# Kernel optimization log

Measured on AMD Instinct MI355X. Metric: run time of the kernel, lower is better.

## Reference

```python
import jax, jax.numpy as jnp
import numpy as np

N_HEADS = 16


def setup_inputs() -> dict:
    key = jax.random.key(0)
    k1, k2, k3 = jax.random.split(key, 3)
    B, T, D = 2, 2048, 1024
    x = jax.random.normal(k1, (B, T, D), dtype=jnp.float32)
    w_qkv = jax.random.normal(k2, (3 * D, D), dtype=jnp.float32) * 0.02
    w_proj = jax.random.normal(k3, (D, D), dtype=jnp.float32) * (0.02 / np.sqrt(24.0))
    return {"x": x, "w_qkv": w_qkv, "w_proj": w_proj}


def reference(x, w_qkv, w_proj):
    B, T, D = x.shape
    H = N_HEADS
    dh = D // H
    # qkv linear (no bias): x @ w_qkv.T -> [B, T, 3D]
    qkv = jnp.einsum('btd,ed->bte', x, w_qkv)
    q, k, v = jnp.split(qkv, 3, axis=-1)
    q = q.reshape(B, T, H, dh)
    k = k.reshape(B, T, H, dh)
    v = v.reshape(B, T, H, dh)
    # attention with materialized scores [B, H, T, S]
    scores = jnp.einsum('bthd,bshd->bhts', q, k) / jnp.sqrt(jnp.asarray(dh, x.dtype))
    attn = jax.nn.softmax(scores.astype(jnp.float32), axis=-1).astype(x.dtype)
    out = jnp.einsum('bhts,bshd->bthd', attn, v).reshape(B, T, D)
    # output projection (no bias)
    return jnp.einsum('btd,ed->bte', out, w_proj)
```

## Files before the change

### kernel.cpp

```cpp
#include <hip/hip_runtime.h>


typedef __attribute__((ext_vector_type(8))) short s8v;
typedef __attribute__((ext_vector_type(8))) unsigned short us8;
typedef __attribute__((ext_vector_type(4))) float f4v;
typedef __attribute__((ext_vector_type(16))) float f16v;

__device__ __forceinline__ unsigned short f2b(float f) {
    unsigned u = __builtin_bit_cast(unsigned, f);
    u += 0x7FFFu + ((u >> 16) & 1u);
    return (unsigned short)(u >> 16);
}
__device__ __forceinline__ unsigned pack2(float a, float b) {
    unsigned ua = __builtin_bit_cast(unsigned, a);
    ua += 0x7FFFu + ((ua >> 16) & 1u);
    unsigned ub = __builtin_bit_cast(unsigned, b);
    ub += 0x7FFFu + ((ub >> 16) & 1u);
    return (ua >> 16) | (ub & 0xFFFF0000u);
}

#if __has_builtin(__builtin_amdgcn_exp2f)
#define EXP2F(x) __builtin_amdgcn_exp2f(x)
#else
#define EXP2F(x) exp2f(x)
#endif

#define QSCALE 0.18033688011112042f

__global__ __launch_bounds__(256) void cvt_all(const float* __restrict__ x,
                                               const float* __restrict__ wq,
                                               const float* __restrict__ wp,
                                               unsigned short* __restrict__ xb,
                                               unsigned short* __restrict__ wqb,
                                               unsigned short* __restrict__ wpb) {
    const int nx = 4096 * 1024 / 4, nq = 3072 * 1024 / 4;
    int i = blockIdx.x * 256 + threadIdx.x;
    const float* s;
    unsigned short* d;
    int j;
    if (i < nx)           { s = x;  d = xb;  j = i; }
    else if (i < nx + nq) { s = wq; d = wqb; j = i - nx; }
    else                  { s = wp; d = wpb; j = i - nx - nq; }
    float4 v = ((const float4*)s)[j];
    ushort4 o;
    o.x = f2b(v.x); o.y = f2b(v.y); o.z = f2b(v.z); o.w = f2b(v.w);
    ((ushort4*)d)[j] = o;
}

#define GLD_LDS16(g, l)                                                                        \
    __builtin_amdgcn_global_load_lds((const __attribute__((address_space(1))) unsigned*)(g),   \
                                     (__attribute__((address_space(3))) unsigned*)(l), 16, 0, 0)

__global__ __launch_bounds__(256) void gemm_qkv(const unsigned short* __restrict__ A,
                                                const unsigned short* __restrict__ B,
                                                unsigned short* __restrict__ qkb,
                                                unsigned short* __restrict__ vtb) {
    __shared__ unsigned short As[128][32];
    __shared__ unsigned short Bs[128][32];
    const int tid = threadIdx.x;
    const int l = tid & 63, w = tid >> 6;
    const int quad = l >> 4, ln = l & 15;
    const int m0 = blockIdx.y * 128, n0 = blockIdx.x * 128;
    const int wm = (w >> 1) * 64, wn = (w & 1) * 64;

    const f4v fz = {0.f, 0.f, 0.f, 0.f};
    f4v acc[4][4];
#pragma unroll
    for (int i = 0; i < 4; ++i)
#pragma unroll
        for (int j = 0; j < 4; ++j) acc[i][j] = fz;

    const int row0 = tid >> 2, kc = tid & 3;
    for (int k0 = 0; k0 < 1024; k0 += 32) {
        GLD_LDS16(A + (size_t)(m0 + row0) * 1024 + k0 + kc * 8, &As[row0][kc * 8]);
        GLD_LDS16(B + (size_t)(n0 + row0) * 1024 + k0 + kc * 8, &Bs[row0][kc * 8]);
        GLD_LDS16(A + (size_t)(m0 + row0 + 64) * 1024 + k0 + kc * 8, &As[row0 + 64][kc * 8]);
        GLD_LDS16(B + (size_t)(n0 + row0 + 64) * 1024 + k0 + kc * 8, &Bs[row0 + 64][kc * 8]);
        __syncthreads();
        s8v af[4], bf[4];
#pragma unroll
        for (int mt = 0; mt < 4; ++mt) af[mt] = *(const s8v*)&As[wm + mt * 16 + ln][quad * 8];
#pragma unroll
        for (int nt = 0; nt < 4; ++nt) bf[nt] = *(const s8v*)&Bs[wn + nt * 16 + ln][quad * 8];
#pragma unroll
        for (int mt = 0; mt < 4; ++mt)
#pragma unroll
            for (int nt = 0; nt < 4; ++nt)
                acc[mt][nt] = __builtin_amdgcn_mfma_f32_16x16x32_bf16(af[mt], bf[nt], acc[mt][nt], 0, 0, 0);
        __syncthreads();
    }

#pragma unroll
    for (int mt = 0; mt < 4; ++mt)
#pragma unroll
        for (int nt = 0; nt < 4; ++nt) {
            const int col = n0 + wn + nt * 16 + ln;
            const int row = m0 + wm + mt * 16 + quad * 4;
            f4v a = acc[mt][nt];
            if (col < 2048) {
                const float sc = (col < 1024) ? QSCALE : 1.0f;
#pragma unroll
                for (int r = 0; r < 4; ++r)
                    qkb[(size_t)(row + r) * 2048 + col] = f2b(a[r] * sc);
            } else {
                const int vd = col - 2048, hh = vd >> 6, dd = vd & 63;
                const int bb = row >> 11, t = row & 2047;
                uint2 pk;
                pk.x = pack2(a[0], a[1]);
                pk.y = pack2(a[2], a[3]);
                *(uint2*)&vtb[((size_t)(bb * 16 + hh) * 64 + dd) * 2048 + t] = pk;
            }
        }
}

__global__ __launch_bounds__(256) void gemm_proj(const unsigned short* __restrict__ A,
                                                 const unsigned short* __restrict__ B,
                                                 float* __restrict__ C) {
    __shared__ unsigned short As[128][32];
    __shared__ unsigned short Bs[64][32];
    const int tid = threadIdx.x;
    const int l = tid & 63, w = tid >> 6;
    const int quad = l >> 4, ln = l & 15;
    const int m0 = blockIdx.y * 128, n0 = blockIdx.x * 64;
    const int wm = w * 32;

    const f4v fz = {0.f, 0.f, 0.f, 0.f};
    f4v acc[2][4];
#pragma unroll
    for (int i = 0; i < 2; ++i)
#pragma unroll
        for (int j = 0; j < 4; ++j) acc[i][j] = fz;

    const int row0 = tid >> 2, kc = tid & 3;
    for (int k0 = 0; k0 < 1024; k0 += 32) {
        GLD_LDS16(A + (size_t)(m0 + row0) * 1024 + k0 + kc * 8, &As[row0][kc * 8]);
        GLD_LDS16(A + (size_t)(m0 + row0 + 64) * 1024 + k0 + kc * 8, &As[row0 + 64][kc * 8]);
        GLD_LDS16(B + (size_t)(n0 + row0) * 1024 + k0 + kc * 8, &Bs[row0][kc * 8]);
        __syncthreads();
        s8v af[2], bf[4];
#pragma unroll
        for (int mt = 0; mt < 2; ++mt) af[mt] = *(const s8v*)&As[wm + mt * 16 + ln][quad * 8];
#pragma unroll
        for (int nt = 0; nt < 4; ++nt) bf[nt] = *(const s8v*)&Bs[nt * 16 + ln][quad * 8];
#pragma unroll
        for (int mt = 0; mt < 2; ++mt)
#pragma unroll
            for (int nt = 0; nt < 4; ++nt)
                acc[mt][nt] = __builtin_amdgcn_mfma_f32_16x16x32_bf16(af[mt], bf[nt], acc[mt][nt], 0, 0, 0);
        __syncthreads();
    }

#pragma unroll
    for (int mt = 0; mt < 2; ++mt)
#pragma unroll
        for (int nt = 0; nt < 4; ++nt) {
            const int row = m0 + wm + mt * 16 + quad * 4;
            const int col = n0 + nt * 16 + ln;
#pragma unroll
            for (int r = 0; r < 4; ++r) C[(size_t)(row + r) * 1024 + col] = acc[mt][nt][r];
        }
}

__global__ __launch_bounds__(256) void attn_mfma(const unsigned short* __restrict__ qkb,
                                                 const unsigned short* __restrict__ vtb,
                                                 unsigned short* __restrict__ attnb) {
    __shared__ unsigned short Qs[128][76];
    __shared__ unsigned short Ks[64][76];
    __shared__ unsigned short Vt[64][76];
    __shared__ unsigned short Ps[128][76];
    __shared__ float lred[128];

    const int tid = threadIdx.x;
    const int l = tid & 63, w = tid >> 6;
    const int m31 = l & 31, h2 = l >> 5;
    const int qw = w * 32;
    const int t0 = blockIdx.x * 128;
    const int hh = blockIdx.y, bb = blockIdx.z;
    const size_t rowbase = (size_t)bb * 2048;
    const unsigned short* Vg = vtb + (size_t)(bb * 16 + hh) * 64 * 2048;

#pragma unroll
    for (int it = 0; it < 4; ++it) {
        const int idx = tid + it * 256;
        const int qr = idx >> 3, qc = (idx & 7) * 8;
        *(us8*)&Qs[qr][qc] = *(const us8*)(qkb + (rowbase + t0 + qr) * 2048 + hh * 64 + qc);
    }

    const int r0 = tid >> 3, c0 = (tid & 7) * 8;

    f16v zz;
#pragma unroll
    for (int i = 0; i < 16; ++i) zz[i] = 0.f;
    f16v oacc[2];
    oacc[0] = zz; oacc[1] = zz;
    float lsum = 0.f;

    us8 kreg0 = *(const us8*)(qkb + (rowbase + r0) * 2048 + 1024 + hh * 64 + c0);
    us8 kreg1 = *(const us8*)(qkb + (rowbase + r0 + 32) * 2048 + 1024 + hh * 64 + c0);
    us8 vreg0 = *(const us8*)(Vg + (size_t)r0 * 2048 + c0);
    us8 vreg1 = *(const us8*)(Vg + (size_t)(r0 + 32) * 2048 + c0);

    for (int s0 = 0; s0 < 2048; s0 += 64) {
        __syncthreads();
        *(us8*)&Ks[r0][c0] = kreg0;
        *(us8*)&Ks[r0 + 32][c0] = kreg1;
        *(us8*)&Vt[r0][c0] = vreg0;
        *(us8*)&Vt[r0 + 32][c0] = vreg1;
        __syncthreads();

        if (s0 + 64 < 2048) {
            const int sn = s0 + 64;
            kreg0 = *(const us8*)(qkb + (rowbase + sn + r0) * 2048 + 1024 + hh * 64 + c0);
            kreg1 = *(const us8*)(qkb + (rowbase + sn + r0 + 32) * 2048 + 1024 + hh * 64 + c0);
            vreg0 = *(const us8*)(Vg + (size_t)r0 * 2048 + sn + c0);
            vreg1 = *(const us8*)(Vg + (size_t)(r0 + 32) * 2048 + sn + c0);
        }

        f16v sacc[2];
        sacc[0] = zz; sacc[1] = zz;
#pragma unroll
        for (int k4 = 0; k4 < 4; ++k4) {
            s8v qf = *(const s8v*)&Qs[qw + m31][k4 * 16 + h2 * 8];
#pragma unroll
            for (int st = 0; st < 2; ++st) {
                s8v kf = *(const s8v*)&Ks[st * 32 + m31][k4 * 16 + h2 * 8];
                sacc[st] = __builtin_amdgcn_mfma_f32_32x32x16_bf16(kf, qf, sacc[st], 0, 0, 0);
            }
        }

#pragma unroll
        for (int st = 0; st < 2; ++st)
#pragma unroll
            for (int g = 0; g < 4; ++g) {
                float p0 = EXP2F(sacc[st][g * 4 + 0]);
                float p1 = EXP2F(sacc[st][g * 4 + 1]);
                float p2 = EXP2F(sacc[st][g * 4 + 2]);
                float p3 = EXP2F(sacc[st][g * 4 + 3]);
                lsum += (p0 + p1) + (p2 + p3);
                uint2 pk;
                pk.x = pack2(p0, p1);
                pk.y = pack2(p2, p3);
                *(uint2*)&Ps[qw + m31][st * 32 + g * 8 + h2 * 4] = pk;
            }

#pragma unroll
        for (int k2 = 0; k2 < 4; ++k2) {
            s8v pf = *(const s8v*)&Ps[qw + m31][k2 * 16 + h2 * 8];
#pragma unroll
            for (int nt = 0; nt < 2; ++nt) {
                s8v vf = *(const s8v*)&Vt[nt * 32 + m31][k2 * 16 + h2 * 8];
                oacc[nt] = __builtin_amdgcn_mfma_f32_32x32x16_bf16(pf, vf, oacc[nt], 0, 0, 0);
            }
        }
    }

    lsum += __shfl_xor(lsum, 32, 64);
    lred[qw + m31] = lsum;
    float inv[16];
#pragma unroll
    for (int g = 0; g < 4; ++g)
#pragma unroll
        for (int r = 0; r < 4; ++r)
            inv[g * 4 + r] = 1.0f / lred[qw + 8 * g + 4 * h2 + r];

#pragma unroll
    for (int nt = 0; nt < 2; ++nt)
#pragma unroll
        for (int g = 0; g < 4; ++g)
#pragma unroll
            for (int r = 0; r < 4; ++r) {
                const int qrow = 8 * g + 4 * h2 + r;
                float o = oacc[nt][g * 4 + r] * inv[g * 4 + r];
                attnb[(rowbase + t0 + qw + qrow) * 1024 + hh * 64 + nt * 32 + m31] = f2b(o);
            }
}

extern "C" void kernel_launch(void* const* d_in, const int* in_sizes, int n_in,
                              void* d_out, int out_size, void* d_ws, size_t ws_size,
                              hipStream_t stream) {
    const float* x      = (const float*)d_in[0];
    const float* w_qkv  = (const float*)d_in[1];
    const float* w_proj = (const float*)d_in[2];
    float* out = (float*)d_out;

    char* p = (char*)d_ws;
    unsigned short* xb    = (unsigned short*)p;  p += (size_t)4096 * 1024 * 2;
    unsigned short* wqb   = (unsigned short*)p;  p += (size_t)3072 * 1024 * 2;
    unsigned short* wpb   = (unsigned short*)p;  p += (size_t)1024 * 1024 * 2;
    unsigned short* qkb   = (unsigned short*)p;  p += (size_t)4096 * 2048 * 2;
    unsigned short* vtb   = (unsigned short*)p;  p += (size_t)2 * 16 * 64 * 2048 * 2;
    unsigned short* attnb = (unsigned short*)p;  p += (size_t)4096 * 1024 * 2;

    cvt_all<<<8192, 256, 0, stream>>>(x, w_qkv, w_proj, xb, wqb, wpb);

    gemm_qkv<<<dim3(3072 / 128, 4096 / 128), 256, 0, stream>>>(xb, wqb, qkb, vtb);

    attn_mfma<<<dim3(2048 / 128, 16, 2), 256, 0, stream>>>(qkb, vtb, attnb);

    gemm_proj<<<dim3(1024 / 64, 4096 / 128), 256, 0, stream>>>(attnb, wpb, out);
}
```

Measured before the change: 209.7 us.

## Load attention K/V fragments directly from global, add separate V transpose kernel

```diff
diff --git a/kernel.cpp b/kernel.cpp
--- a/kernel.cpp
+++ b/kernel.cpp
@@ -11,12 +11,12 @@
     u += 0x7FFFu + ((u >> 16) & 1u);
     return (unsigned short)(u >> 16);
 }
-__device__ __forceinline__ unsigned pack2(float a, float b) {
-    unsigned ua = __builtin_bit_cast(unsigned, a);
-    ua += 0x7FFFu + ((ua >> 16) & 1u);
-    unsigned ub = __builtin_bit_cast(unsigned, b);
-    ub += 0x7FFFu + ((ub >> 16) & 1u);
-    return (ua >> 16) | (ub & 0xFFFF0000u);
+__device__ __forceinline__ unsigned packtrunc(float a, float b, unsigned sel) {
+    unsigned r;
+    asm("v_perm_b32 %0, %1, %2, %3"
+        : "=v"(r)
+        : "v"(__builtin_bit_cast(unsigned, b)), "v"(__builtin_bit_cast(unsigned, a)), "s"(sel));
+    return r;
 }
 
 #if __has_builtin(__builtin_amdgcn_exp2f)
@@ -53,8 +53,7 @@
 
 __global__ __launch_bounds__(256) void gemm_qkv(const unsigned short* __restrict__ A,
                                                 const unsigned short* __restrict__ B,
-                                                unsigned short* __restrict__ qkb,
-                                                unsigned short* __restrict__ vtb) {
+                                                unsigned short* __restrict__ qkvb) {
     __shared__ unsigned short As[128][32];
     __shared__ unsigned short Bs[128][32];
     const int tid = threadIdx.x;
@@ -96,21 +95,36 @@
         for (int nt = 0; nt < 4; ++nt) {
             const int col = n0 + wn + nt * 16 + ln;
             const int row = m0 + wm + mt * 16 + quad * 4;
-            f4v a = acc[mt][nt];
-            if (col < 2048) {
-                const float sc = (col < 1024) ? QSCALE : 1.0f;
-#pragma unroll
-                for (int r = 0; r < 4; ++r)
-                    qkb[(size_t)(row + r) * 2048 + col] = f2b(a[r] * sc);
-            } else {
-                const int vd = col - 2048, hh = vd >> 6, dd = vd & 63;
-                const int bb = row >> 11, t = row & 2047;
-                uint2 pk;
-                pk.x = pack2(a[0], a[1]);
-                pk.y = pack2(a[2], a[3]);
-                *(uint2*)&vtb[((size_t)(bb * 16 + hh) * 64 + dd) * 2048 + t] = pk;
-            }
+            const float sc = (col < 1024) ? QSCALE : 1.0f;
+#pragma unroll
+            for (int r = 0; r < 4; ++r)
+                qkvb[(size_t)(row + r) * 3072 + col] = f2b(acc[mt][nt][r] * sc);
         }
+}
+
+__global__ __launch_bounds__(256) void vtrans(const unsigned short* __restrict__ qkvb,
+                                              unsigned short* __restrict__ vtb) {
+    __shared__ unsigned Ls[64][65];
+    const int tid = threadIdx.x;
+    const int t0 = blockIdx.x * 64, h = blockIdx.y, b = blockIdx.z;
+#pragma unroll
+    for (int it = 0; it < 2; ++it) {
+        int idx = tid + it * 256;
+        int r = idx >> 3, c8 = idx & 7;
+        us8 v = *(const us8*)(qkvb + ((size_t)b * 2048 + t0 + r) * 3072 + 2048 + h * 64 + c8 * 8);
+#pragma unroll
+        for (int j = 0; j < 8; ++j) Ls[r][c8 * 8 + j] = v[j];
+    }
+    __syncthreads();
+#pragma unroll
+    for (int it = 0; it < 2; ++it) {
+        int idx = tid + it * 256;
+        int d = idx >> 3, tc = idx & 7;
+        us8 o;
+#pragma unroll
+        for (int j = 0; j < 8; ++j) o[j] = (unsigned short)Ls[tc * 8 + j][d];
+        *(us8*)(vtb + ((size_t)(b * 16 + h) * 64 + d) * 2048 + t0 + tc * 8) = o;
+    }
 }
 
 __global__ __launch_bounds__(256) void gemm_proj(const unsigned short* __restrict__ A,
@@ -161,12 +175,9 @@
         }
 }
 
-__global__ __launch_bounds__(256) void attn_mfma(const unsigned short* __restrict__ qkb,
+__global__ __launch_bounds__(256) void attn_mfma(const unsigned short* __restrict__ qkvb,
                                                  const unsigned short* __restrict__ vtb,
                                                  unsigned short* __restrict__ attnb) {
-    __shared__ unsigned short Qs[128][76];
-    __shared__ unsigned short Ks[64][76];
-    __shared__ unsigned short Vt[64][76];
     __shared__ unsigned short Ps[128][76];
     __shared__ float lred[128];
 
@@ -177,16 +188,15 @@
     const int t0 = blockIdx.x * 128;
     const int hh = blockIdx.y, bb = blockIdx.z;
     const size_t rowbase = (size_t)bb * 2048;
-    const unsigned short* Vg = vtb + (size_t)(bb * 16 + hh) * 64 * 2048;
-
-#pragma unroll
-    for (int it = 0; it < 4; ++it) {
-        const int idx = tid + it * 256;
-        const int qr = idx >> 3, qc = (idx & 7) * 8;
-        *(us8*)&Qs[qr][qc] = *(const us8*)(qkb + (rowbase + t0 + qr) * 2048 + hh * 64 + qc);
-    }
-
-    const int r0 = tid >> 3, c0 = (tid & 7) * 8;
+    const unsigned sel = 0x07060302u;
+
+    const unsigned short* Qg = qkvb + (rowbase + t0 + qw + m31) * 3072 + hh * 64 + h2 * 8;
+    const unsigned short* Kg = qkvb + (rowbase + m31) * 3072 + 1024 + hh * 64 + h2 * 8;
+    const unsigned short* Vg = vtb + ((size_t)(bb * 16 + hh) * 64 + m31) * 2048 + h2 * 8;
+
+    s8v qf[4];
+#pragma unroll
+    for (int k4 = 0; k4 < 4; ++k4) qf[k4] = *(const s8v*)(Qg + k4 * 16);
 
     f16v zz;
 #pragma unroll
@@ -195,38 +205,27 @@
     oacc[0] = zz; oacc[1] = zz;
     float lsum = 0.f;
 
-    us8 kreg0 = *(const us8*)(qkb + (rowbase + r0) * 2048 + 1024 + hh * 64 + c0);
-    us8 kreg1 = *(const us8*)(qkb + (rowbase + r0 + 32) * 2048 + 1024 + hh * 64 + c0);
-    us8 vreg0 = *(const us8*)(Vg + (size_t)r0 * 2048 + c0);
-    us8 vreg1 = *(const us8*)(Vg + (size_t)(r0 + 32) * 2048 + c0);
-
     for (int s0 = 0; s0 < 2048; s0 += 64) {
-        __syncthreads();
-        *(us8*)&Ks[r0][c0] = kreg0;
-        *(us8*)&Ks[r0 + 32][c0] = kreg1;
-        *(us8*)&Vt[r0][c0] = vreg0;
-        *(us8*)&Vt[r0 + 32][c0] = vreg1;
-        __syncthreads();
-
-        if (s0 + 64 < 2048) {
-            const int sn = s0 + 64;
-            kreg0 = *(const us8*)(qkb + (rowbase + sn + r0) * 2048 + 1024 + hh * 64 + c0);
-            kreg1 = *(const us8*)(qkb + (rowbase + sn + r0 + 32) * 2048 + 1024 + hh * 64 + c0);
-            vreg0 = *(const us8*)(Vg + (size_t)r0 * 2048 + sn + c0);
-            vreg1 = *(const us8*)(Vg + (size_t)(r0 + 32) * 2048 + sn + c0);
-        }
+        s8v kf[2][4];
+#pragma unroll
+        for (int st = 0; st < 2; ++st)
+#pragma unroll
+            for (int k4 = 0; k4 < 4; ++k4)
+                kf[st][k4] = *(const s8v*)(Kg + (size_t)(s0 + st * 32) * 3072 + k4 * 16);
+        s8v vf[2][4];
+#pragma unroll
+        for (int nt = 0; nt < 2; ++nt)
+#pragma unroll
+            for (int k2 = 0; k2 < 4; ++k2)
+                vf[nt][k2] = *(const s8v*)(Vg + (size_t)(nt * 32) * 2048 + s0 + k2 * 16);
 
         f16v sacc[2];
         sacc[0] = zz; sacc[1] = zz;
 #pragma unroll
-        for (int k4 = 0; k4 < 4; ++k4) {
-            s8v qf = *(const s8v*)&Qs[qw + m31][k4 * 16 + h2 * 8];
-#pragma unroll
-            for (int st = 0; st < 2; ++st) {
-                s8v kf = *(const s8v*)&Ks[st * 32 + m31][k4 * 16 + h2 * 8];
-                sacc[st] = __builtin_amdgcn_mfma_f32_32x32x16_bf16(kf, qf, sacc[st], 0, 0, 0);
-            }
-        }
+        for (int k4 = 0; k4 < 4; ++k4)
+#pragma unroll
+            for (int st = 0; st < 2; ++st)
+                sacc[st] = __builtin_amdgcn_mfma_f32_32x32x16_bf16(kf[st][k4], qf[k4], sacc[st], 0, 0, 0);
 
 #pragma unroll
         for (int st = 0; st < 2; ++st)
@@ -238,8 +237,8 @@
                 float p3 = EXP2F(sacc[st][g * 4 + 3]);
                 lsum += (p0 + p1) + (p2 + p3);
                 uint2 pk;
-                pk.x = pack2(p0, p1);
-                pk.y = pack2(p2, p3);
+                pk.x = packtrunc(p0, p1, sel);
+                pk.y = packtrunc(p2, p3, sel);
                 *(uint2*)&Ps[qw + m31][st * 32 + g * 8 + h2 * 4] = pk;
             }
 
@@ -247,10 +246,8 @@
         for (int k2 = 0; k2 < 4; ++k2) {
             s8v pf = *(const s8v*)&Ps[qw + m31][k2 * 16 + h2 * 8];
 #pragma unroll
-            for (int nt = 0; nt < 2; ++nt) {
-                s8v vf = *(const s8v*)&Vt[nt * 32 + m31][k2 * 16 + h2 * 8];
-                oacc[nt] = __builtin_amdgcn_mfma_f32_32x32x16_bf16(pf, vf, oacc[nt], 0, 0, 0);
-            }
+            for (int nt = 0; nt < 2; ++nt)
+                oacc[nt] = __builtin_amdgcn_mfma_f32_32x32x16_bf16(pf, vf[nt][k2], oacc[nt], 0, 0, 0);
         }
     }
 
@@ -261,7 +258,7 @@
     for (int g = 0; g < 4; ++g)
 #pragma unroll
         for (int r = 0; r < 4; ++r)
-            inv[g * 4 + r] = 1.0f / lred[qw + 8 * g + 4 * h2 + r];
+            inv[g * 4 + r] = 1.001955f / lred[qw + 8 * g + 4 * h2 + r];
 
 #pragma unroll
     for (int nt = 0; nt < 2; ++nt)
@@ -287,15 +284,17 @@
     unsigned short* xb    = (unsigned short*)p;  p += (size_t)4096 * 1024 * 2;
     unsigned short* wqb   = (unsigned short*)p;  p += (size_t)3072 * 1024 * 2;
     unsigned short* wpb   = (unsigned short*)p;  p += (size_t)1024 * 1024 * 2;
-    unsigned short* qkb   = (unsigned short*)p;  p += (size_t)4096 * 2048 * 2;
+    unsigned short* qkvb  = (unsigned short*)p;  p += (size_t)4096 * 3072 * 2;
     unsigned short* vtb   = (unsigned short*)p;  p += (size_t)2 * 16 * 64 * 2048 * 2;
     unsigned short* attnb = (unsigned short*)p;  p += (size_t)4096 * 1024 * 2;
 
     cvt_all<<<8192, 256, 0, stream>>>(x, w_qkv, w_proj, xb, wqb, wpb);
 
-    gemm_qkv<<<dim3(3072 / 128, 4096 / 128), 256, 0, stream>>>(xb, wqb, qkb, vtb);
-
-    attn_mfma<<<dim3(2048 / 128, 16, 2), 256, 0, stream>>>(qkb, vtb, attnb);
+    gemm_qkv<<<dim3(3072 / 128, 4096 / 128), 256, 0, stream>>>(xb, wqb, qkvb);
+
+    vtrans<<<dim3(32, 16, 2), 256, 0, stream>>>(qkvb, vtb);
+
+    attn_mfma<<<dim3(2048 / 128, 16, 2), 256, 0, stream>>>(qkvb, vtb, attnb);
 
     gemm_proj<<<dim3(1024 / 64, 4096 / 128), 256, 0, stream>>>(attnb, wpb, out);
 }
```

Measured after the change: 255.4 us. +21.8%, slower.
